# Kernel optimization log

Hardware: AMD Instinct MI355X
Metric: run time of the kernel (lower is better)

Reference implementation:

```python
import jax, jax.numpy as jnp
import numpy as np

N_NODES = 100000
N_EDGES = 1600000


def _glorot(key, shape):
    lim = float(np.sqrt(6.0 / (shape[0] + shape[1])))
    return jax.random.uniform(key, shape, jnp.float32, -lim, lim)


def setup_inputs() -> dict:
    key = jax.random.key(0)
    ks = jax.random.split(key, 12)
    x = jax.random.normal(ks[0], (N_NODES, 8), jnp.float32)
    edge_index = jax.random.randint(ks[1], (2, N_EDGES), 0, N_NODES, jnp.int64)
    dims = [(8, 32), (32, 32), (32, 32), (32, 32), (32, 3)]
    params = {}
    for i, (din, dout) in enumerate(dims):
        params[f"W{i+1}"] = _glorot(ks[2 + i], (din, dout))
        params[f"b{i+1}"] = jnp.zeros((dout,), jnp.float32)
    return {"x": x, "edge_index": edge_index, **params}


def _gcn_norm(edge_index, num_nodes):
    # add self-loops, symmetric normalization (PyG GCNConv defaults)
    loops = jnp.arange(num_nodes, dtype=edge_index.dtype)
    row = jnp.concatenate([edge_index[0], loops])
    col = jnp.concatenate([edge_index[1], loops])
    deg = jax.ops.segment_sum(jnp.ones_like(col, jnp.float32), col,
                              num_segments=num_nodes)
    dinv = jnp.where(deg > 0, jax.lax.rsqrt(deg), 0.0)
    norm = dinv[row] * dinv[col]  # [E + N]
    return row, col, norm


def _gcn_conv(h, W, b, row, col, norm, num_nodes):
    h = h @ W                                   # [N, dout]
    msg = h[row] * norm[:, None]                # gather + scale
    out = jax.ops.segment_sum(msg, col, num_segments=num_nodes)
    return out + b


def reference(x, edge_index, W1, b1, W2, b2, W3, b3, W4, b4, W5, b5):
    row, col, norm = _gcn_norm(edge_index, N_NODES)
    lrelu = lambda h: jax.nn.leaky_relu(h, negative_slope=1.0)  # identity, kept faithful
    h = lrelu(_gcn_conv(x, W1, b1, row, col, norm, N_NODES))
    h = lrelu(_gcn_conv(h, W2, b2, row, col, norm, N_NODES))
    h = lrelu(_gcn_conv(h, W3, b3, row, col, norm, N_NODES))
    h = lrelu(_gcn_conv(h, W4, b4, row, col, norm, N_NODES))
    h = lrelu(_gcn_conv(h, W5, b5, row, col, norm, N_NODES))
    return h
```

## Files before the change

### kernel.cpp

```cpp
#include <hip/hip_runtime.h>

#define NN 100000
#define NE 1600000
#define NB 391
#define EPB 3125
#define NBLK 512
#define CAP 4608



__global__ __launch_bounds__(512) void bucket_scatter_kernel(const void* __restrict__ ei,
                                                             int* __restrict__ bcursor,
                                                             unsigned int* __restrict__ epacked) {
    __shared__ int lcount[NB];
    __shared__ int lcur[NB];
    int tid = threadIdx.x;
    for (int i = tid; i < NB; i += 512) lcount[i] = 0;
    int base = blockIdx.x * EPB;
    unsigned int hw = ((const unsigned int*)ei)[2 * (base + tid) + 1];
    int is64 = (__ballot(hw != 0) == 0ULL);
    int r[7], c[7];
    r[6] = -1;
    if (!is64) {
        const int* e32 = (const int*)ei;
#pragma unroll
        for (int k = 0; k < 6; k++) {
            int e = base + k * 512 + tid;
            r[k] = e32[e];
            c[k] = e32[NE + e];
        }
        if (tid < EPB - 6 * 512) {
            int e = base + 6 * 512 + tid;
            r[6] = e32[e];
            c[6] = e32[NE + e];
        }
    } else {
        const long long* e64 = (const long long*)ei;
#pragma unroll
        for (int k = 0; k < 6; k++) {
            int e = base + k * 512 + tid;
            r[k] = (int)e64[e];
            c[k] = (int)e64[(long long)NE + e];
        }
        if (tid < EPB - 6 * 512) {
            int e = base + 6 * 512 + tid;
            r[6] = (int)e64[e];
            c[6] = (int)e64[(long long)NE + e];
        }
    }
    __syncthreads();
#pragma unroll
    for (int k = 0; k < 7; k++)
        if (r[k] >= 0) atomicAdd(&lcount[c[k] >> 8], 1);
    __syncthreads();
    for (int i = tid; i < NB; i += 512) {
        int cnt = lcount[i];
        lcur[i] = (cnt ? atomicAdd(&bcursor[i], cnt) : 0) + i * CAP;
    }
    __syncthreads();
#pragma unroll
    for (int k = 0; k < 7; k++) {
        if (r[k] >= 0) {
            int b = c[k] >> 8;
            int pos = atomicAdd(&lcur[b], 1);
            if (pos < (b + 1) * CAP)
                epacked[pos] = ((unsigned)(c[k] & 255) << 24) | (unsigned)r[k];
        }
    }
}


__global__ __launch_bounds__(512) void bucket_csr_kernel(
    const unsigned int* __restrict__ epacked, const int* __restrict__ bcount,
    const float* __restrict__ x,
    const float* __restrict__ W1, const float* __restrict__ b1,
    const float* __restrict__ W2, const float* __restrict__ b2,
    const float* __restrict__ W3, const float* __restrict__ b3,
    const float* __restrict__ W4, const float* __restrict__ b4,
    const float* __restrict__ W5, const float* __restrict__ b5,
    float* __restrict__ cv,
    int2* __restrict__ meta, int* __restrict__ srow,
    float4* __restrict__ Ta, int N) {
    __shared__ float w45[96], w345[96], w2345[96];
    __shared__ float4 Wl4[8];
    __shared__ int lcount[256];
    __shared__ int lcur[256];
    __shared__ int wsum[4];
    __shared__ int sbuf[CAP];
    int b = blockIdx.x;
    int tid = threadIdx.x;
    int s0 = b * CAP;
    int cnt = bcount[b];
    if (cnt > CAP) cnt = CAP;
    if (tid < 256) lcount[tid] = 0;
    int i3 = tid / 3, j3 = tid - 3 * (tid / 3);
    if (tid < 96) {
        float s = 0.0f;
        for (int k = 0; k < 32; k++) s += W4[i3 * 32 + k] * W5[k * 3 + j3];
        w45[i3 * 3 + j3] = s;
    }
    __syncthreads();
    unsigned int ev[9];
#pragma unroll
    for (int k = 0; k < 9; k++) {
        int i = k * 512 + tid;
        ev[k] = (i < cnt) ? epacked[s0 + i] : 0xFFFFFFFFu;
    }
    if (tid < 96) {
        float s = 0.0f;
        for (int k = 0; k < 32; k++) s += W3[i3 * 32 + k] * w45[k * 3 + j3];
        w345[i3 * 3 + j3] = s;
    }
    __syncthreads();
    if (tid < 96) {
        float s = 0.0f;
        for (int k = 0; k < 32; k++) s += W2[i3 * 32 + k] * w345[k * 3 + j3];
        w2345[i3 * 3 + j3] = s;
    }
    __syncthreads();
    if (tid < 32) {
        int ii = tid >> 2, jj = tid & 3;
        float s = 0.0f;
        if (jj < 3)
            for (int k = 0; k < 32; k++) s += W1[ii * 32 + k] * w2345[k * 3 + jj];
        ((float*)Wl4)[tid] = s;
    }
    if (b == 0 && tid >= 32 && tid < 52) {
        int kk = (tid - 32) >> 2, jj = (tid - 32) & 3;
        float s = 0.0f;
        if (jj < 3) {
            if (kk == 0) for (int k = 0; k < 32; k++) s += b1[k] * w2345[k * 3 + jj];
            if (kk == 1) for (int k = 0; k < 32; k++) s += b2[k] * w345[k * 3 + jj];
            if (kk == 2) for (int k = 0; k < 32; k++) s += b3[k] * w45[k * 3 + jj];
            if (kk == 3) for (int k = 0; k < 32; k++) s += b4[k] * W5[k * 3 + jj];
            if (kk == 4) s = b5[jj];
        }
        cv[tid - 32] = s;
    }
#pragma unroll
    for (int k = 0; k < 9; k++)
        if (ev[k] != 0xFFFFFFFFu) atomicAdd(&lcount[ev[k] >> 24], 1);
    __syncthreads();
    int lane = tid & 63, w = tid >> 6;
    int myc = (tid < 256) ? lcount[tid] : 0;
    int acc = myc;
#pragma unroll
    for (int off = 1; off < 64; off <<= 1) {
        int y = __shfl_up(acc, off);
        if (lane >= off) acc += y;
    }
    if (lane == 63 && w < 4) wsum[w] = acc;
    __syncthreads();
    if (tid == 0) {
        int s = 0;
#pragma unroll
        for (int j = 0; j < 4; j++) { int t = wsum[j]; wsum[j] = s; s += t; }
    }
    __syncthreads();
    if (tid < 256) {
        int excl = acc - myc + wsum[w];
        lcur[tid] = excl;
        int col = (b << 8) + tid;
        if (col < N) {
            meta[col] = make_int2(s0 + excl, myc);
            float d = 1.0f / sqrtf((float)myc + 1.0f);
            const float4* x4 = (const float4*)x + col * 2;
            float4 av = x4[0], bv = x4[1];
            float xs[8] = {av.x, av.y, av.z, av.w, bv.x, bv.y, bv.z, bv.w};
            float4 o = make_float4(0.f, 0.f, 0.f, 0.f);
#pragma unroll
            for (int k = 0; k < 8; k++) {
                float4 ww = Wl4[k];
                o.x += xs[k] * ww.x; o.y += xs[k] * ww.y; o.z += xs[k] * ww.z;
            }
            o.x *= d; o.y *= d; o.z *= d; o.w = 0.0f;
            Ta[col] = o;
        }
    }
    __syncthreads();
#pragma unroll
    for (int k = 0; k < 9; k++) {
        if (ev[k] != 0xFFFFFFFFu) {
            int p = atomicAdd(&lcur[ev[k] >> 24], 1);
            sbuf[p] = (int)(ev[k] & 0xFFFFFFu);
        }
    }
    __syncthreads();
    for (int i = tid; i < cnt; i += 512) srow[s0 + i] = sbuf[i];
}


template <bool LAST>
__global__ __launch_bounds__(256) void prop_kernel(
    const int2* __restrict__ meta, const int* __restrict__ srow,
    const float4* __restrict__ tin, const float* __restrict__ cv, int k,
    float4* __restrict__ tout, float* __restrict__ out, int N) {
    int tid = blockIdx.x * 256 + threadIdx.x;
    int c = tid >> 2, q = tid & 3;
    if (c >= N) return;
    int2 m = meta[c];
    int s = m.x;
    int d = m.y;
    float4 a = (q == 0) ? tin[c] : make_float4(0.f, 0.f, 0.f, 0.f);
    float4 a2 = make_float4(0.f, 0.f, 0.f, 0.f);
    int i = q;
    for (; i + 4 < d; i += 8) {
        int r0 = srow[s + i];
        int r1 = srow[s + i + 4];
        float4 v0 = tin[r0];
        float4 v1 = tin[r1];
        a.x += v0.x; a.y += v0.y; a.z += v0.z;
        a2.x += v1.x; a2.y += v1.y; a2.z += v1.z;
    }
    if (i < d) {
        float4 v = tin[srow[s + i]];
        a.x += v.x; a.y += v.y; a.z += v.z;
    }
    a.x += a2.x; a.y += a2.y; a.z += a2.z;
    a.x += __shfl_xor(a.x, 1); a.y += __shfl_xor(a.y, 1); a.z += __shfl_xor(a.z, 1);
    a.x += __shfl_xor(a.x, 2); a.y += __shfl_xor(a.y, 2); a.z += __shfl_xor(a.z, 2);
    if (q == 0) {
        float dd = 1.0f / sqrtf((float)d + 1.0f);
        float cx = cv[k * 4 + 0], cy = cv[k * 4 + 1], cz = cv[k * 4 + 2];
        if (LAST) {
            out[c * 3 + 0] = dd * a.x + cx;
            out[c * 3 + 1] = dd * a.y + cy;
            out[c * 3 + 2] = dd * a.z + cz;
        } else {
            float d2 = dd * dd;
            float4 o;
            o.x = d2 * a.x + dd * cx;
            o.y = d2 * a.y + dd * cy;
            o.z = d2 * a.z + dd * cz;
            o.w = 0.0f;
            tout[c] = o;
        }
    }
}


extern "C" void kernel_launch(void* const* d_in, const int* in_sizes, int n_in,
                              void* d_out, int out_size, void* d_ws, size_t ws_size,
                              hipStream_t stream) {
    const float* x  = (const float*)d_in[0];
    const void*  ei = d_in[1];
    const float* W1 = (const float*)d_in[2];  const float* b1 = (const float*)d_in[3];
    const float* W2 = (const float*)d_in[4];  const float* b2 = (const float*)d_in[5];
    const float* W3 = (const float*)d_in[6];  const float* b3 = (const float*)d_in[7];
    const float* W4 = (const float*)d_in[8];  const float* b4 = (const float*)d_in[9];
    const float* W5 = (const float*)d_in[10]; const float* b5 = (const float*)d_in[11];
    float* out = (float*)d_out;

    char* p = (char*)d_ws;
    auto alloc = [&](size_t bytes) {
        char* r = p;
        p += (bytes + 255) & ~(size_t)255;
        return r;
    };
    int2*  meta    = (int2*)alloc((size_t)NN * 8);
    int*   bcursor = (int*)alloc(NB * 4);
    float* cv      = (float*)alloc(5 * 4 * 4);
    unsigned int* epacked = (unsigned int*)alloc((size_t)NB * CAP * 4);
    int*          srow    = (int*)alloc((size_t)NB * CAP * 4);
    float4*       Ta      = (float4*)alloc((size_t)NN * 16);
    float4*       Tb      = (float4*)alloc((size_t)NN * 16);
    if ((size_t)(p - (char*)d_ws) > ws_size) return;

    hipMemsetAsync(bcursor, 0, NB * 4, stream);
    bucket_scatter_kernel<<<NBLK, 512, 0, stream>>>(ei, bcursor, epacked);
    bucket_csr_kernel<<<NB, 512, 0, stream>>>(epacked, bcursor, x,
                                              W1, b1, W2, b2, W3, b3, W4, b4, W5, b5,
                                              cv, meta, srow, Ta, NN);

    int gP = (NN * 4 + 255) / 256;
    prop_kernel<false><<<gP, 256, 0, stream>>>(meta, srow, Ta, cv, 0, Tb, nullptr, NN);
    prop_kernel<false><<<gP, 256, 0, stream>>>(meta, srow, Tb, cv, 1, Ta, nullptr, NN);
    prop_kernel<false><<<gP, 256, 0, stream>>>(meta, srow, Ta, cv, 2, Tb, nullptr, NN);
    prop_kernel<false><<<gP, 256, 0, stream>>>(meta, srow, Tb, cv, 3, Ta, nullptr, NN);
    prop_kernel<true><<<gP, 256, 0, stream>>>(meta, srow, Ta, cv, 4, nullptr, out, NN);
}
```

Measured before the change: 173.3 us.

## Pad per-node CSR segments to multiples of four for int4 index loads

Each node's neighbour list in the bucketed CSR is padded to a multiple of four entries, filled with a dummy index pointing at an extra zero row appended to both feature buffers. The propagation kernel then reads neighbour indices as aligned int4 vectors and issues four independent gathers per iteration with four accumulators, replacing scalar index loads and the tail branch. The cost is a larger per-bucket capacity, a shared-memory fill of the padding, and some wasted gathers of the zero row for low-degree nodes.

```diff
diff --git a/kernel.cpp b/kernel.cpp
--- a/kernel.cpp
+++ b/kernel.cpp
@@ -5,7 +5,8 @@
 #define NB 391
 #define EPB 3125
 #define NBLK 512
-#define CAP 4608
+#define CAP 5632
+#define RCAP 4608
 
 
 
@@ -63,7 +64,7 @@
         if (r[k] >= 0) {
             int b = c[k] >> 8;
             int pos = atomicAdd(&lcur[b], 1);
-            if (pos < (b + 1) * CAP)
+            if (pos < b * CAP + RCAP)
                 epacked[pos] = ((unsigned)(c[k] & 255) << 24) | (unsigned)r[k];
         }
     }
@@ -80,19 +81,21 @@
     const float* __restrict__ W5, const float* __restrict__ b5,
     float* __restrict__ cv,
     int2* __restrict__ meta, int* __restrict__ srow,
-    float4* __restrict__ Ta, int N) {
+    float4* __restrict__ Ta, float4* __restrict__ Tb, int N) {
     __shared__ float w45[96], w345[96], w2345[96];
     __shared__ float4 Wl4[8];
     __shared__ int lcount[256];
     __shared__ int lcur[256];
     __shared__ int wsum[4];
+    __shared__ int ptot;
     __shared__ int sbuf[CAP];
     int b = blockIdx.x;
     int tid = threadIdx.x;
     int s0 = b * CAP;
     int cnt = bcount[b];
-    if (cnt > CAP) cnt = CAP;
+    if (cnt > RCAP) cnt = RCAP;
     if (tid < 256) lcount[tid] = 0;
+    for (int i = tid; i < CAP; i += 512) sbuf[i] = NN;
     int i3 = tid / 3, j3 = tid - 3 * (tid / 3);
     if (tid < 96) {
         float s = 0.0f;
@@ -137,13 +140,18 @@
         }
         cv[tid - 32] = s;
     }
+    if (b == 0 && tid == 52) {
+        Ta[NN] = make_float4(0.f, 0.f, 0.f, 0.f);
+        Tb[NN] = make_float4(0.f, 0.f, 0.f, 0.f);
+    }
 #pragma unroll
     for (int k = 0; k < 9; k++)
         if (ev[k] != 0xFFFFFFFFu) atomicAdd(&lcount[ev[k] >> 24], 1);
     __syncthreads();
     int lane = tid & 63, w = tid >> 6;
     int myc = (tid < 256) ? lcount[tid] : 0;
-    int acc = myc;
+    int myp = (myc + 3) & ~3;
+    int acc = myp;
 #pragma unroll
     for (int off = 1; off < 64; off <<= 1) {
         int y = __shfl_up(acc, off);
@@ -158,8 +166,9 @@
     }
     __syncthreads();
     if (tid < 256) {
-        int excl = acc - myc + wsum[w];
+        int excl = acc - myp + wsum[w];
         lcur[tid] = excl;
+        if (tid == 255) ptot = excl + myp;
         int col = (b << 8) + tid;
         if (col < N) {
             meta[col] = make_int2(s0 + excl, myc);
@@ -186,7 +195,8 @@
         }
     }
     __syncthreads();
-    for (int i = tid; i < cnt; i += 512) srow[s0 + i] = sbuf[i];
+    int pt = ptot;
+    for (int i = tid; i < pt; i += 512) srow[s0 + i] = sbuf[i];
 }
 
 
@@ -201,37 +211,41 @@
     int2 m = meta[c];
     int s = m.x;
     int d = m.y;
-    float4 a = (q == 0) ? tin[c] : make_float4(0.f, 0.f, 0.f, 0.f);
-    float4 a2 = make_float4(0.f, 0.f, 0.f, 0.f);
-    int i = q;
-    for (; i + 4 < d; i += 8) {
-        int r0 = srow[s + i];
-        int r1 = srow[s + i + 4];
-        float4 v0 = tin[r0];
-        float4 v1 = tin[r1];
-        a.x += v0.x; a.y += v0.y; a.z += v0.z;
-        a2.x += v1.x; a2.y += v1.y; a2.z += v1.z;
-    }
-    if (i < d) {
-        float4 v = tin[srow[s + i]];
-        a.x += v.x; a.y += v.y; a.z += v.z;
-    }
-    a.x += a2.x; a.y += a2.y; a.z += a2.z;
-    a.x += __shfl_xor(a.x, 1); a.y += __shfl_xor(a.y, 1); a.z += __shfl_xor(a.z, 1);
-    a.x += __shfl_xor(a.x, 2); a.y += __shfl_xor(a.y, 2); a.z += __shfl_xor(a.z, 2);
+    int dpad = (d + 3) & ~3;
+    float ax = 0.f, ay = 0.f, az = 0.f;
+    if (q == 0) { float4 t = tin[c]; ax = t.x; ay = t.y; az = t.z; }
+    float bx = 0.f, by = 0.f, bz = 0.f;
+    float cx = 0.f, cy = 0.f, cz = 0.f;
+    float dx = 0.f, dy = 0.f, dz = 0.f;
+    for (int j = 4 * q; j < dpad; j += 16) {
+        int4 rr = *(const int4*)(srow + s + j);
+        float4 v0 = tin[rr.x];
+        float4 v1 = tin[rr.y];
+        float4 v2 = tin[rr.z];
+        float4 v3 = tin[rr.w];
+        ax += v0.x; ay += v0.y; az += v0.z;
+        bx += v1.x; by += v1.y; bz += v1.z;
+        cx += v2.x; cy += v2.y; cz += v2.z;
+        dx += v3.x; dy += v3.y; dz += v3.z;
+    }
+    ax += bx + cx + dx;
+    ay += by + cy + dy;
+    az += bz + cz + dz;
+    ax += __shfl_xor(ax, 1); ay += __shfl_xor(ay, 1); az += __shfl_xor(az, 1);
+    ax += __shfl_xor(ax, 2); ay += __shfl_xor(ay, 2); az += __shfl_xor(az, 2);
     if (q == 0) {
         float dd = 1.0f / sqrtf((float)d + 1.0f);
-        float cx = cv[k * 4 + 0], cy = cv[k * 4 + 1], cz = cv[k * 4 + 2];
+        float vx = cv[k * 4 + 0], vy = cv[k * 4 + 1], vz = cv[k * 4 + 2];
         if (LAST) {
-            out[c * 3 + 0] = dd * a.x + cx;
-            out[c * 3 + 1] = dd * a.y + cy;
-            out[c * 3 + 2] = dd * a.z + cz;
+            out[c * 3 + 0] = dd * ax + vx;
+            out[c * 3 + 1] = dd * ay + vy;
+            out[c * 3 + 2] = dd * az + vz;
         } else {
             float d2 = dd * dd;
             float4 o;
-            o.x = d2 * a.x + dd * cx;
-            o.y = d2 * a.y + dd * cy;
-            o.z = d2 * a.z + dd * cz;
+            o.x = d2 * ax + dd * vx;
+            o.y = d2 * ay + dd * vy;
+            o.z = d2 * az + dd * vz;
             o.w = 0.0f;
             tout[c] = o;
         }
@@ -262,15 +276,15 @@
     float* cv      = (float*)alloc(5 * 4 * 4);
     unsigned int* epacked = (unsigned int*)alloc((size_t)NB * CAP * 4);
     int*          srow    = (int*)alloc((size_t)NB * CAP * 4);
-    float4*       Ta      = (float4*)alloc((size_t)NN * 16);
-    float4*       Tb      = (float4*)alloc((size_t)NN * 16);
+    float4*       Ta      = (float4*)alloc((size_t)(NN + 1) * 16);
+    float4*       Tb      = (float4*)alloc((size_t)(NN + 1) * 16);
     if ((size_t)(p - (char*)d_ws) > ws_size) return;
 
     hipMemsetAsync(bcursor, 0, NB * 4, stream);
     bucket_scatter_kernel<<<NBLK, 512, 0, stream>>>(ei, bcursor, epacked);
     bucket_csr_kernel<<<NB, 512, 0, stream>>>(epacked, bcursor, x,
                                               W1, b1, W2, b2, W3, b3, W4, b4, W5, b5,
-                                              cv, meta, srow, Ta, NN);
+                                              cv, meta, srow, Ta, Tb, NN);
 
     int gP = (NN * 4 + 255) / 256;
     prop_kernel<false><<<gP, 256, 0, stream>>>(meta, srow, Ta, cv, 0, Tb, nullptr, NN);
```

Result: no change. 171.0 us (-1.3%).
